# Kernel tuning notes

Hardware: AMD Instinct MI355X
Metric: run time of the kernel (lower is better)

Reference implementation:

```python
import jax, jax.numpy as jnp
import numpy as np

H = 12           # num_heads
D_MODEL = 768
SCALE = (D_MODEL // H) ** -0.5  # qk_scale default: head_dim**-0.5


def _attn_mask(q, k, v, mask):
    # sim: (b, i, j); mask broadcast over query dim (mask.unsqueeze(1) in torch)
    sim = jnp.einsum('bid,bjd->bij', q, k) + mask[:, None, :]
    a = jax.nn.softmax(sim, axis=-1)
    return jnp.einsum('bij,bjd->bid', a, v)


def setup_inputs() -> dict:
    key = jax.random.key(0)
    k0, k1, k2, k3 = jax.random.split(key, 4)
    B, F, n, D = 16, 8, 196, 768
    N = 1 + F * n  # cls + frames*patches = 1569
    x = jax.random.normal(k0, (B, N, D), jnp.float32)
    x_mask = jax.random.normal(k1, (B, N), jnp.float32)  # additive attention mask
    Wqkv = jax.random.normal(k2, (3 * D, D), jnp.float32) * (D ** -0.5)
    Wproj = jax.random.normal(k3, (D, D), jnp.float32) * (D ** -0.5)
    bproj = jnp.zeros((D,), jnp.float32)
    return {"x": x, "x_mask": x_mask, "Wqkv": Wqkv, "Wproj": Wproj,
            "bproj": bproj, "f": F}


def reference(x, x_mask, Wqkv, Wproj, bproj, f):
    B, N, D = x.shape
    h = H
    d = D // h
    # qkv projection (qkv_bias=False), split into q,k,v
    qkv = x @ Wqkv.T                       # (B, N, 3D)
    q, k, v = jnp.split(qkv, 3, axis=-1)

    def to_heads(t):  # 'b n (h d) -> (b h) n d'
        return t.reshape(B, N, h, d).transpose(0, 2, 1, 3).reshape(B * h, N, d)

    q, k, v = map(to_heads, (q, k, v))
    mask = jnp.repeat(x_mask, h, axis=0)   # repeat_interleave over heads: (B*h, N)

    q = q * SCALE
    cls_q, q_ = q[:, :1], q[:, 1:]
    cls_k, k_ = k[:, :1], k[:, 1:]
    cls_v, v_ = v[:, :1], v[:, 1:]
    cls_mask, mask_ = mask[:, :1], mask[:, 1:]

    # cls token attends to everything
    cls_out = _attn_mask(cls_q, k, v, mask)            # (B*h, 1, d)

    # spatial attention: 'b (f n) d -> (b f) n d'
    n = (N - 1) // f
    q_ = q_.reshape(B * h * f, n, d)
    k_ = k_.reshape(B * h * f, n, d)
    v_ = v_.reshape(B * h * f, n, d)
    mask_ = mask_.reshape(B * h * f, n)

    # prepend cls k/v/mask to every frame group (r = f)
    cls_k = jnp.repeat(cls_k, f, axis=0)               # (B*h*f, 1, d)
    cls_v = jnp.repeat(cls_v, f, axis=0)
    cls_m = jnp.repeat(cls_mask, f, axis=0)            # (B*h*f, 1)
    k_ = jnp.concatenate([cls_k, k_], axis=1)          # (B*h*f, n+1, d)
    v_ = jnp.concatenate([cls_v, v_], axis=1)
    m2 = jnp.concatenate([cls_m, mask_], axis=1)       # (B*h*f, n+1)

    out = _attn_mask(q_, k_, v_, m2)                   # (B*h*f, n, d)
    out = out.reshape(B * h, f * n, d)                 # '(b f) n d -> b (f n) d'
    out = jnp.concatenate([cls_out, out], axis=1)      # (B*h, N, d)
    out = out.reshape(B, h, N, d).transpose(0, 2, 1, 3).reshape(B, N, D)
    return out @ Wproj.T + bproj
```

## Files before the change

### kernel.cpp

```cpp
#include <hip/hip_runtime.h>
#include <hip/hip_bf16.h>
#include <stdint.h>

#define Hh 12
#define Dm 768
#define Bb 16
#define Nt 1569
#define Ff 8
#define NC 196
#define BH 192
#define Mr 25104
#define CPW 224
#define VTW (8*CPW)
#define PLD 232
#define CLD 132

typedef __attribute__((ext_vector_type(8))) short bf16x8;
typedef __attribute__((ext_vector_type(4))) float f32x4;

typedef const __attribute__((address_space(1))) uint32_t guint;
typedef __attribute__((address_space(3))) uint32_t luint;

static __device__ __forceinline__ float bf2f(unsigned short u) {
  union { unsigned int i; float f; } v; v.i = ((unsigned int)u) << 16; return v.f;
}
static __device__ __forceinline__ unsigned short f2bf(float f) {
  __hip_bfloat16 h = __float2bfloat16(f);
  return __builtin_bit_cast(unsigned short, h);
}

__global__ void cast3_k(const float4* __restrict__ s0, ushort4* __restrict__ d0, int n0,
                        const float4* __restrict__ s1, ushort4* __restrict__ d1, int n1,
                        const float4* __restrict__ s2, ushort4* __restrict__ d2, int n2) {
  int nTot = n0 + n1 + n2;
  for (int i = blockIdx.x * blockDim.x + threadIdx.x; i < nTot; i += gridDim.x * blockDim.x) {
    const float4* s; ushort4* d; int off;
    if (i < n0) { s = s0; d = d0; off = i; }
    else if (i < n0 + n1) { s = s1; d = d1; off = i - n0; }
    else { s = s2; d = d2; off = i - n0 - n1; }
    float4 f = s[off];
    ushort4 u;
    u.x = f2bf(f.x); u.y = f2bf(f.y); u.z = f2bf(f.z); u.w = f2bf(f.w);
    d[off] = u;
  }
}

template<int MODE>
__global__ __launch_bounds__(256) void gemm_k(
    const __hip_bfloat16* __restrict__ A,
    const __hip_bfloat16* __restrict__ W,
    int M, int K,
    __hip_bfloat16* __restrict__ qh, __hip_bfloat16* __restrict__ kh,
    __hip_bfloat16* __restrict__ vT, __hip_bfloat16* __restrict__ vcls,
    const float* __restrict__ bias, float* __restrict__ outp)
{
  __shared__ __align__(16) unsigned short shmem[128 * CLD];
  unsigned short* ls0 = shmem;
  unsigned short* ls1 = shmem + 4096;
  unsigned short* ls2 = shmem + 8192;
  unsigned short* ls3 = shmem + 12288;

  const int tid = threadIdx.x;
  const int lane = tid & 63, wid = tid >> 6;
  const int waveM = wid >> 1, waveN = wid & 1;

  const int gridN = gridDim.x;
  const int nwg = gridDim.x * gridDim.y;
  int bid = blockIdx.y * gridN + blockIdx.x;
  int q8 = nwg >> 3, r8 = nwg & 7;
  int xcd = bid & 7, lid = bid >> 3;
  int swz = (xcd < r8 ? xcd * (q8 + 1) : r8 * (q8 + 1) + (xcd - r8) * q8) + lid;
  const int mBase = (swz / gridN) * 128, nBase = (swz % gridN) * 128;

  const int l15 = lane & 15, lg = lane >> 4;
  f32x4 acc[4][4] = {};
  const int nkt = K >> 6;
  for (int kt = 0; kt < nkt; ++kt) {
#pragma unroll
    for (int s = 0; s < 2; ++s) {
      int seg = s * 256 + tid;
      int row = seg >> 2, ks = seg & 3;
      int arow = mBase + row; if (arow >= M) arow = M - 1;
      int brow = nBase + row;
      const __hip_bfloat16* ap = A + (size_t)arow * K + kt * 64 + ks * 8;
      const __hip_bfloat16* wp = W + (size_t)brow * K + kt * 64 + ks * 8;
      __builtin_amdgcn_global_load_lds((guint*)ap,        (luint*)&ls0[seg * 8], 16, 0, 0);
      __builtin_amdgcn_global_load_lds((guint*)wp,        (luint*)&ls1[seg * 8], 16, 0, 0);
      __builtin_amdgcn_global_load_lds((guint*)(ap + 32), (luint*)&ls2[seg * 8], 16, 0, 0);
      __builtin_amdgcn_global_load_lds((guint*)(wp + 32), (luint*)&ls3[seg * 8], 16, 0, 0);
    }
    __syncthreads();
    bf16x8 aF[4], bF[4], aG[4], bG[4];
#pragma unroll
    for (int i = 0; i < 4; ++i) {
      int ro = (waveM * 64 + i * 16 + l15) * 32 + lg * 8;
      int co = (waveN * 64 + i * 16 + l15) * 32 + lg * 8;
      aF[i] = *reinterpret_cast<const bf16x8*>(&ls0[ro]);
      bF[i] = *reinterpret_cast<const bf16x8*>(&ls1[co]);
      aG[i] = *reinterpret_cast<const bf16x8*>(&ls2[ro]);
      bG[i] = *reinterpret_cast<const bf16x8*>(&ls3[co]);
    }
#pragma unroll
    for (int mi = 0; mi < 4; ++mi)
#pragma unroll
      for (int ni = 0; ni < 4; ++ni) {
        acc[mi][ni] = __builtin_amdgcn_mfma_f32_16x16x32_bf16(aF[mi], bF[ni], acc[mi][ni], 0, 0, 0);
        acc[mi][ni] = __builtin_amdgcn_mfma_f32_16x16x32_bf16(aG[mi], bG[ni], acc[mi][ni], 0, 0, 0);
      }
    __syncthreads();
  }

  if (MODE == 1) {
    const bool fullM = (mBase + 128 <= M);
#pragma unroll
    for (int mi = 0; mi < 4; ++mi)
#pragma unroll
      for (int ni = 0; ni < 4; ++ni)
#pragma unroll
        for (int r = 0; r < 4; ++r) {
          int grow = mBase + waveM * 64 + mi * 16 + lg * 4 + r;
          if (!fullM && grow >= M) continue;
          int gcol = nBase + waveN * 64 + ni * 16 + l15;
          outp[(size_t)grow * Dm + gcol] = acc[mi][ni][r] + bias[gcol];
        }
    return;
  }

  const int which = nBase / Dm;
  const int headBase = (nBase - which * Dm) >> 6;
  const float scl = (which == 0) ? 0.125f : 1.f;
  const bool fullM = (mBase + 128 <= M);

  if (fullM) {
    if (which < 2) {
#pragma unroll
      for (int mi = 0; mi < 4; ++mi)
#pragma unroll
        for (int ni = 0; ni < 4; ++ni)
#pragma unroll
          for (int r = 0; r < 4; ++r)
            shmem[(waveM * 64 + mi * 16 + lg * 4 + r) * CLD + (waveN * 64 + ni * 16 + l15)]
                = f2bf(acc[mi][ni][r] * scl);
      __syncthreads();
      __hip_bfloat16* dst = (which == 0) ? qh : kh;
      int row = tid >> 1, h = tid & 1;
      int grow = mBase + row;
      int b = grow / Nt, i = grow - b * Nt;
      const uint2* sp = reinterpret_cast<const uint2*>(&shmem[row * CLD + h * 64]);
      uint2* dp = reinterpret_cast<uint2*>(
          dst + ((size_t)(b * Hh + headBase + h) * Nt + i) * 64);
#pragma unroll
      for (int j = 0; j < 16; ++j) dp[j] = sp[j];
    } else {
#pragma unroll
      for (int mi = 0; mi < 4; ++mi)
#pragma unroll
        for (int ni = 0; ni < 4; ++ni)
#pragma unroll
          for (int r = 0; r < 4; ++r)
            shmem[(waveN * 64 + ni * 16 + l15) * CLD + (waveM * 64 + mi * 16 + lg * 4 + r)]
                = f2bf(acc[mi][ni][r]);
      __syncthreads();
      int lc = tid & 127, rhalf = tid >> 7;
      int h = lc >> 6, dc = lc & 63;
      int head = headBase + h;
#pragma unroll
      for (int g = 0; g < 8; ++g) {
        int row0 = rhalf * 64 + g * 8;
        int grow0 = mBase + row0;
        int b = grow0 / Nt, i0 = grow0 - b * Nt;
        const unsigned short* sp = &shmem[lc * CLD + row0];
        if (i0 >= 1 && i0 + 8 <= Nt) {
          int j0 = i0 - 1, cc = j0 / NC, key = j0 - cc * NC;
          if (key + 8 <= NC) {
            int bh = b * Hh + head;
            __hip_bfloat16* p = vT + ((size_t)bh * 64 + dc) * VTW + cc * CPW + key;
            if ((key & 1) == 0) {
              const unsigned int* s4 = reinterpret_cast<const unsigned int*>(sp);
              unsigned int* d4 = reinterpret_cast<unsigned int*>(p);
              d4[0] = s4[0]; d4[1] = s4[1]; d4[2] = s4[2]; d4[3] = s4[3];
            } else {
#pragma unroll
              for (int j = 0; j < 8; ++j)
                p[j] = __builtin_bit_cast(__hip_bfloat16, sp[j]);
            }
            continue;
          }
        }
#pragma unroll
        for (int j = 0; j < 8; ++j) {
          int grow = grow0 + j;
          int bb = grow / Nt, ii = grow - bb * Nt;
          int bh2 = bb * Hh + head;
          unsigned short val = sp[j];
          if (ii == 0) {
            vcls[bh2 * 64 + dc] = __builtin_bit_cast(__hip_bfloat16, val);
          } else {
            int jj = ii - 1, cc2 = jj / NC, k2 = jj - cc2 * NC;
            vT[((size_t)bh2 * 64 + dc) * VTW + cc2 * CPW + k2]
                = __builtin_bit_cast(__hip_bfloat16, val);
          }
        }
      }
    }
  } else {
#pragma unroll
    for (int mi = 0; mi < 4; ++mi)
#pragma unroll
      for (int ni = 0; ni < 4; ++ni)
#pragma unroll
        for (int r = 0; r < 4; ++r) {
          int grow = mBase + waveM * 64 + mi * 16 + lg * 4 + r;
          if (grow >= M) continue;
          int gcol = nBase + waveN * 64 + ni * 16 + l15;
          float v = acc[mi][ni][r];
          int b = grow / Nt, i = grow - b * Nt;
          int hcol = gcol - which * Dm;
          int head = hcol >> 6, dc = hcol & 63;
          int bh = b * Hh + head;
          if (which == 0) {
            qh[((size_t)bh * Nt + i) * 64 + dc] = __float2bfloat16(v * 0.125f);
          } else if (which == 1) {
            kh[((size_t)bh * Nt + i) * 64 + dc] = __float2bfloat16(v);
          } else {
            if (i == 0) vcls[bh * 64 + dc] = __float2bfloat16(v);
            else {
              int j = i - 1; int cc = j / NC, key = j - cc * NC;
              vT[((size_t)bh * 64 + dc) * VTW + cc * CPW + key] = __float2bfloat16(v);
            }
          }
        }
  }
}

__global__ __launch_bounds__(256, 2) void attn_k(
    const __hip_bfloat16* __restrict__ qh, const __hip_bfloat16* __restrict__ kh,
    const __hip_bfloat16* __restrict__ vT, const __hip_bfloat16* __restrict__ vcls,
    const float* __restrict__ x_mask, __hip_bfloat16* __restrict__ ao)
{
  __shared__ __align__(16) char smem[56320];

  const int bidx = blockIdx.x;
  const int tid = threadIdx.x;

  if (bidx < BH) {
    float* sS = reinterpret_cast<float*>(smem);
    float* qv = reinterpret_cast<float*>(smem + 6400);
    float* red = reinterpret_cast<float*>(smem + 6656);
    const int bh = bidx, b = bh / Hh, head = bh - b * Hh;
    if (tid < 64) qv[tid] = __bfloat162float(qh[((size_t)bh * Nt) * 64 + tid]);
    __syncthreads();
    float lmax = -1e30f;
    for (int j = tid; j < Nt; j += 256) {
      const __hip_bfloat16* kr = kh + ((size_t)bh * Nt + j) * 64;
      float dot = 0.f;
#pragma unroll
      for (int d0 = 0; d0 < 64; d0 += 8) {
        bf16x8 kv = *reinterpret_cast<const bf16x8*>(kr + d0);
#pragma unroll
        for (int i = 0; i < 8; ++i) dot += qv[d0 + i] * bf2f((unsigned short)kv[i]);
      }
      float s = dot + x_mask[b * Nt + j];
      sS[j] = s;
      lmax = fmaxf(lmax, s);
    }
    red[tid] = lmax; __syncthreads();
    for (int off = 128; off > 0; off >>= 1) {
      if (tid < off) red[tid] = fmaxf(red[tid], red[tid + off]);
      __syncthreads();
    }
    float m = red[0]; __syncthreads();
    float lsum = 0.f;
    for (int j = tid; j < Nt; j += 256) { float e = __expf(sS[j] - m); sS[j] = e; lsum += e; }
    red[tid] = lsum; __syncthreads();
    for (int off = 128; off > 0; off >>= 1) {
      if (tid < off) red[tid] += red[tid + off];
      __syncthreads();
    }
    float rden = 1.f / red[0]; __syncthreads();
    int dc = tid & 63, part = tid >> 6;
    float partial = 0.f;
    if (part == 0) partial = sS[0] * __bfloat162float(vcls[bh * 64 + dc]);
    const __hip_bfloat16* vrow = vT + ((size_t)bh * 64 + dc) * VTW;
    for (int cc = part * 2; cc < part * 2 + 2; ++cc) {
      int base = 1 + cc * NC;
      const __hip_bfloat16* vc2 = vrow + cc * CPW;
      int key = 0;
      for (; key + 8 <= NC; key += 8) {
        bf16x8 vv = *reinterpret_cast<const bf16x8*>(vc2 + key);
#pragma unroll
        for (int i = 0; i < 8; ++i)
          partial += sS[base + key + i] * bf2f((unsigned short)vv[i]);
      }
      for (; key < NC; ++key)
        partial += sS[base + key] * __bfloat162float(vc2[key]);
    }
    red[tid] = partial; __syncthreads();
    if (tid < 64) {
      float o = (red[tid] + red[tid + 64] + red[tid + 128] + red[tid + 192]) * rden;
      ao[((size_t)b * Nt) * Dm + head * 64 + dc] = __float2bfloat16(o);
    }
    return;
  }

  __hip_bfloat16* ldsK = reinterpret_cast<__hip_bfloat16*>(smem);
  __hip_bfloat16* ldsP = reinterpret_cast<__hip_bfloat16*>(smem + 26624);

  const int g = bidx - BH;
  const int bh = g >> 3, c = g & 7;
  const int b = bh / Hh, head = bh - b * Hh;
  const int lane = tid & 63, wid = tid >> 6;
  const int l15 = lane & 15, lg = lane >> 4;

  const int kbase = 1 + c * NC;

#pragma unroll
  for (int it = 0; it < 7; ++it) {
    int idx = it * 256 + tid;
    if (idx < 1664) {
      int row = idx >> 3, c16 = idx & 7;
      int token = kbase + row; if (token > Nt - 1) token = Nt - 1;
      __builtin_amdgcn_global_load_lds(
          (guint*)(kh + ((size_t)bh * Nt + token) * 64 + ((c16 ^ (row & 7)) * 8)),
          (luint*)&ldsK[idx * 8], 16, 0, 0);
    }
  }
  __syncthreads();

  __hip_bfloat16* myP = ldsP + wid * (16 * PLD);

  const __hip_bfloat16* kc = kh + (size_t)bh * Nt * 64;
  bf16x8 ck0 = *reinterpret_cast<const bf16x8*>(kc + lg * 8);
  bf16x8 ck1 = *reinterpret_cast<const bf16x8*>(kc + 32 + lg * 8);
  const float maskCls = x_mask[b * Nt];

  for (int rt = wid; rt < 13; rt += 4) {
    int qlrow = rt * 16 + l15;
    int qtok = 1 + c * NC + qlrow; if (qtok > Nt - 1) qtok = Nt - 1;
    const __hip_bfloat16* qp = qh + ((size_t)bh * Nt + qtok) * 64;
    bf16x8 aQ0 = *reinterpret_cast<const bf16x8*>(qp + lg * 8);
    bf16x8 aQ1 = *reinterpret_cast<const bf16x8*>(qp + 32 + lg * 8);

    float pc0 = 0.f;
#pragma unroll
    for (int i = 0; i < 8; ++i)
      pc0 += bf2f((unsigned short)aQ0[i]) * bf2f((unsigned short)ck0[i])
           + bf2f((unsigned short)aQ1[i]) * bf2f((unsigned short)ck1[i]);
    pc0 += __shfl_xor(pc0, 16);
    pc0 += __shfl_xor(pc0, 32);
    pc0 += maskCls;

    f32x4 S[13];
    float mv[13];
#define LD_MM(i) { \
    int row = (i) * 16 + l15; \
    bf16x8 kb0 = *reinterpret_cast<const bf16x8*>(&ldsK[row * 64 + ((lg ^ (l15 & 7)) * 8)]); \
    bf16x8 kb1 = *reinterpret_cast<const bf16x8*>(&ldsK[row * 64 + (((4 + lg) ^ (l15 & 7)) * 8)]); \
    mv[i] = (row < NC) ? x_mask[b * Nt + kbase + row] : -1e30f; \
    f32x4 sa = {}; \
    sa = __builtin_amdgcn_mfma_f32_16x16x32_bf16(aQ0, kb0, sa, 0, 0, 0); \
    sa = __builtin_amdgcn_mfma_f32_16x16x32_bf16(aQ1, kb1, sa, 0, 0, 0); \
    S[i][0] = sa[0] + mv[i]; S[i][1] = sa[1] + mv[i]; \
    S[i][2] = sa[2] + mv[i]; S[i][3] = sa[3] + mv[i]; }
    LD_MM(0) LD_MM(1) LD_MM(2) LD_MM(3) LD_MM(4) LD_MM(5) LD_MM(6)
    LD_MM(7) LD_MM(8) LD_MM(9) LD_MM(10) LD_MM(11) LD_MM(12)
#undef LD_MM

    float pcls[4], rden[4];
#pragma unroll
    for (int r = 0; r < 4; ++r) {
      float m = -1e30f;
#pragma unroll
      for (int nt = 0; nt < 13; ++nt) m = fmaxf(m, S[nt][r]);
      m = fmaxf(m, __shfl_xor(m, 1));
      m = fmaxf(m, __shfl_xor(m, 2));
      m = fmaxf(m, __shfl_xor(m, 4));
      m = fmaxf(m, __shfl_xor(m, 8));
      float sc = __shfl(pc0, lg * 4 + r);
      m = fmaxf(m, sc);
      float sum = 0.f;
#pragma unroll
      for (int nt = 0; nt < 13; ++nt) { float e = __expf(S[nt][r] - m); S[nt][r] = e; sum += e; }
      sum += __shfl_xor(sum, 1);
      sum += __shfl_xor(sum, 2);
      sum += __shfl_xor(sum, 4);
      sum += __shfl_xor(sum, 8);
      float pc = __expf(sc - m);
      pcls[r] = pc;
      rden[r] = 1.f / (sum + pc);
    }

#pragma unroll
    for (int nt = 0; nt < 13; ++nt)
#pragma unroll
      for (int r = 0; r < 4; ++r)
        myP[(lg * 4 + r) * PLD + nt * 16 + l15] = __float2bfloat16(S[nt][r]);
#pragma unroll
    for (int r = 0; r < 4; ++r)
      myP[l15 * PLD + 208 + lg * 4 + r] = __float2bfloat16(0.f);
    asm volatile("s_waitcnt lgkmcnt(0)" ::: "memory");
    __builtin_amdgcn_sched_barrier(0);

    f32x4 O[4] = {};
#define PVK(kt) { \
    bf16x8 aP = *reinterpret_cast<const bf16x8*>(&myP[l15 * PLD + (kt) * 32 + lg * 8]); \
    { int dc = 0 * 16 + l15; bf16x8 bV = *reinterpret_cast<const bf16x8*>(vT + ((size_t)bh * 64 + dc) * VTW + c * CPW + (kt) * 32 + lg * 8); \
      O[0] = __builtin_amdgcn_mfma_f32_16x16x32_bf16(aP, bV, O[0], 0, 0, 0); } \
    { int dc = 1 * 16 + l15; bf16x8 bV = *reinterpret_cast<const bf16x8*>(vT + ((size_t)bh * 64 + dc) * VTW + c * CPW + (kt) * 32 + lg * 8); \
      O[1] = __builtin_amdgcn_mfma_f32_16x16x32_bf16(aP, bV, O[1], 0, 0, 0); } \
    { int dc = 2 * 16 + l15; bf16x8 bV = *reinterpret_cast<const bf16x8*>(vT + ((size_t)bh * 64 + dc) * VTW + c * CPW + (kt) * 32 + lg * 8); \
      O[2] = __builtin_amdgcn_mfma_f32_16x16x32_bf16(aP, bV, O[2], 0, 0, 0); } \
    { int dc = 3 * 16 + l15; bf16x8 bV = *reinterpret_cast<const bf16x8*>(vT + ((size_t)bh * 64 + dc) * VTW + c * CPW + (kt) * 32 + lg * 8); \
      O[3] = __builtin_amdgcn_mfma_f32_16x16x32_bf16(aP, bV, O[3], 0, 0, 0); } }
    PVK(0) PVK(1) PVK(2) PVK(3) PVK(4) PVK(5) PVK(6)
#undef PVK

#pragma unroll
    for (int ni = 0; ni < 4; ++ni) {
      int dc = ni * 16 + l15;
      float vc = __bfloat162float(vcls[bh * 64 + dc]);
#pragma unroll
      for (int r = 0; r < 4; ++r) {
        int lrow = rt * 16 + lg * 4 + r;
        if (lrow < NC) {
          float o = (O[ni][r] + pcls[r] * vc) * rden[r];
          int tok = 1 + c * NC + lrow;
          ao[((size_t)b * Nt + tok) * Dm + head * 64 + dc] = __float2bfloat16(o);
        }
      }
    }
  }
}

extern "C" void kernel_launch(void* const* d_in, const int* in_sizes, int n_in,
                              void* d_out, int out_size, void* d_ws, size_t ws_size,
                              hipStream_t stream) {
  const float* x     = (const float*)d_in[0];
  const float* xmask = (const float*)d_in[1];
  const float* wqkv  = (const float*)d_in[2];
  const float* wproj = (const float*)d_in[3];
  const float* bproj = (const float*)d_in[4];
  float* outp = (float*)d_out;

  char* ws = (char*)d_ws;
  size_t off = 0;
  auto alloc = [&](size_t bytes) {
    char* p = ws + off;
    off += (bytes + 255) & ~(size_t)255;
    return p;
  };
  __hip_bfloat16* xb     = (__hip_bfloat16*)alloc((size_t)Mr * Dm * 2);
  __hip_bfloat16* wqkvb  = (__hip_bfloat16*)alloc((size_t)3 * Dm * Dm * 2);
  __hip_bfloat16* wprojb = (__hip_bfloat16*)alloc((size_t)Dm * Dm * 2);
  __hip_bfloat16* qh     = (__hip_bfloat16*)alloc((size_t)BH * Nt * 64 * 2);
  __hip_bfloat16* kh     = (__hip_bfloat16*)alloc((size_t)BH * Nt * 64 * 2);
  __hip_bfloat16* vT     = (__hip_bfloat16*)alloc((size_t)BH * 64 * VTW * 2);
  __hip_bfloat16* vcls   = (__hip_bfloat16*)alloc((size_t)BH * 64 * 2);
  __hip_bfloat16* ao = xb;

  cast3_k<<<2048, 256, 0, stream>>>((const float4*)x, (ushort4*)xb, Mr * Dm / 4,
                                    (const float4*)wqkv, (ushort4*)wqkvb, 3 * Dm * Dm / 4,
                                    (const float4*)wproj, (ushort4*)wprojb, Dm * Dm / 4);

  gemm_k<0><<<dim3(18, 197), 256, 0, stream>>>(xb, wqkvb, Mr, Dm, qh, kh, vT, vcls, nullptr, nullptr);

  attn_k<<<BH + BH * Ff, 256, 0, stream>>>(qh, kh, vT, vcls, xmask, ao);

  gemm_k<1><<<dim3(6, 197), 256, 0, stream>>>(ao, wprojb, Mr, Dm, nullptr, nullptr, nullptr, nullptr, bproj, outp);
}
```

Baseline: 351.9 us.

## Stage V tile in swizzled LDS and widen attention blocks to 512 threads

The attention kernel now runs 512 threads per block (8 waves), so the 13 query row tiles per frame group are spread over 8 waves instead of 4, and the CLS path reduces over 8 partial groups. Each block also copies its frame's V^T tile (64 x 224) into LDS with an XOR swizzle, and the PV MFMA B-operand loads read from LDS instead of global memory. This aims to raise parallelism per block and remove repeated global loads of V across waves. In exchange, LDS per block grows to about 116 KB, which likely allows only one block per CU. Waves 5-7 get a single row tile while the others get two, leaving the work unbalanced.

```diff
diff --git a/kernel.cpp b/kernel.cpp
--- a/kernel.cpp
+++ b/kernel.cpp
@@ -233,12 +233,12 @@
   }
 }
 
-__global__ __launch_bounds__(256, 2) void attn_k(
+__global__ __launch_bounds__(512, 2) void attn_k(
     const __hip_bfloat16* __restrict__ qh, const __hip_bfloat16* __restrict__ kh,
     const __hip_bfloat16* __restrict__ vT, const __hip_bfloat16* __restrict__ vcls,
     const float* __restrict__ x_mask, __hip_bfloat16* __restrict__ ao)
 {
-  __shared__ __align__(16) char smem[56320];
+  __shared__ __align__(16) char smem[118784];
 
   const int bidx = blockIdx.x;
   const int tid = threadIdx.x;
@@ -251,7 +251,7 @@
     if (tid < 64) qv[tid] = __bfloat162float(qh[((size_t)bh * Nt) * 64 + tid]);
     __syncthreads();
     float lmax = -1e30f;
-    for (int j = tid; j < Nt; j += 256) {
+    for (int j = tid; j < Nt; j += 512) {
       const __hip_bfloat16* kr = kh + ((size_t)bh * Nt + j) * 64;
       float dot = 0.f;
 #pragma unroll
@@ -265,15 +265,15 @@
       lmax = fmaxf(lmax, s);
     }
     red[tid] = lmax; __syncthreads();
-    for (int off = 128; off > 0; off >>= 1) {
+    for (int off = 256; off > 0; off >>= 1) {
       if (tid < off) red[tid] = fmaxf(red[tid], red[tid + off]);
       __syncthreads();
     }
     float m = red[0]; __syncthreads();
     float lsum = 0.f;
-    for (int j = tid; j < Nt; j += 256) { float e = __expf(sS[j] - m); sS[j] = e; lsum += e; }
+    for (int j = tid; j < Nt; j += 512) { float e = __expf(sS[j] - m); sS[j] = e; lsum += e; }
     red[tid] = lsum; __syncthreads();
-    for (int off = 128; off > 0; off >>= 1) {
+    for (int off = 256; off > 0; off >>= 1) {
       if (tid < off) red[tid] += red[tid + off];
       __syncthreads();
     }
@@ -281,10 +281,9 @@
     int dc = tid & 63, part = tid >> 6;
     float partial = 0.f;
     if (part == 0) partial = sS[0] * __bfloat162float(vcls[bh * 64 + dc]);
-    const __hip_bfloat16* vrow = vT + ((size_t)bh * 64 + dc) * VTW;
-    for (int cc = part * 2; cc < part * 2 + 2; ++cc) {
-      int base = 1 + cc * NC;
-      const __hip_bfloat16* vc2 = vrow + cc * CPW;
+    {
+      int base = 1 + part * NC;
+      const __hip_bfloat16* vc2 = vT + ((size_t)bh * 64 + dc) * VTW + part * CPW;
       int key = 0;
       for (; key + 8 <= NC; key += 8) {
         bf16x8 vv = *reinterpret_cast<const bf16x8*>(vc2 + key);
@@ -297,14 +296,17 @@
     }
     red[tid] = partial; __syncthreads();
     if (tid < 64) {
-      float o = (red[tid] + red[tid + 64] + red[tid + 128] + red[tid + 192]) * rden;
-      ao[((size_t)b * Nt) * Dm + head * 64 + dc] = __float2bfloat16(o);
+      float o = 0.f;
+#pragma unroll
+      for (int k = 0; k < 8; ++k) o += red[tid + 64 * k];
+      ao[((size_t)b * Nt) * Dm + head * 64 + dc] = __float2bfloat16(o * rden);
     }
     return;
   }
 
   __hip_bfloat16* ldsK = reinterpret_cast<__hip_bfloat16*>(smem);
-  __hip_bfloat16* ldsP = reinterpret_cast<__hip_bfloat16*>(smem + 26624);
+  __hip_bfloat16* ldsV = reinterpret_cast<__hip_bfloat16*>(smem + 26624);
+  __hip_bfloat16* ldsP = reinterpret_cast<__hip_bfloat16*>(smem + 59392);
 
   const int g = bidx - BH;
   const int bh = g >> 3, c = g & 7;
@@ -315,8 +317,8 @@
   const int kbase = 1 + c * NC;
 
 #pragma unroll
-  for (int it = 0; it < 7; ++it) {
-    int idx = it * 256 + tid;
+  for (int it = 0; it < 4; ++it) {
+    int idx = it * 512 + tid;
     if (idx < 1664) {
       int row = idx >> 3, c16 = idx & 7;
       int token = kbase + row; if (token > Nt - 1) token = Nt - 1;
@@ -325,6 +327,16 @@
           (luint*)&ldsK[idx * 8], 16, 0, 0);
     }
   }
+#pragma unroll
+  for (int it = 0; it < 4; ++it) {
+    int idx = it * 512 + tid;
+    if (idx < 1792) {
+      int dc = idx / 28, u = idx - dc * 28;
+      uint4 v = *reinterpret_cast<const uint4*>(
+          vT + ((size_t)bh * 64 + dc) * VTW + c * CPW + u * 8);
+      *reinterpret_cast<uint4*>(&ldsV[dc * 256 + ((u ^ (dc & 7)) * 8)]) = v;
+    }
+  }
   __syncthreads();
 
   __hip_bfloat16* myP = ldsP + wid * (16 * PLD);
@@ -334,7 +346,7 @@
   bf16x8 ck1 = *reinterpret_cast<const bf16x8*>(kc + 32 + lg * 8);
   const float maskCls = x_mask[b * Nt];
 
-  for (int rt = wid; rt < 13; rt += 4) {
+  for (int rt = wid; rt < 13; rt += 8) {
     int qlrow = rt * 16 + l15;
     int qtok = 1 + c * NC + qlrow; if (qtok > Nt - 1) qtok = Nt - 1;
     const __hip_bfloat16* qp = qh + ((size_t)bh * Nt + qtok) * 64;
@@ -404,13 +416,13 @@
     f32x4 O[4] = {};
 #define PVK(kt) { \
     bf16x8 aP = *reinterpret_cast<const bf16x8*>(&myP[l15 * PLD + (kt) * 32 + lg * 8]); \
-    { int dc = 0 * 16 + l15; bf16x8 bV = *reinterpret_cast<const bf16x8*>(vT + ((size_t)bh * 64 + dc) * VTW + c * CPW + (kt) * 32 + lg * 8); \
+    { int dc = 0 * 16 + l15; bf16x8 bV = *reinterpret_cast<const bf16x8*>(&ldsV[dc * 256 + ((((kt) * 4 + lg) ^ (l15 & 7)) * 8)]); \
       O[0] = __builtin_amdgcn_mfma_f32_16x16x32_bf16(aP, bV, O[0], 0, 0, 0); } \
-    { int dc = 1 * 16 + l15; bf16x8 bV = *reinterpret_cast<const bf16x8*>(vT + ((size_t)bh * 64 + dc) * VTW + c * CPW + (kt) * 32 + lg * 8); \
+    { int dc = 1 * 16 + l15; bf16x8 bV = *reinterpret_cast<const bf16x8*>(&ldsV[dc * 256 + ((((kt) * 4 + lg) ^ (l15 & 7)) * 8)]); \
       O[1] = __builtin_amdgcn_mfma_f32_16x16x32_bf16(aP, bV, O[1], 0, 0, 0); } \
-    { int dc = 2 * 16 + l15; bf16x8 bV = *reinterpret_cast<const bf16x8*>(vT + ((size_t)bh * 64 + dc) * VTW + c * CPW + (kt) * 32 + lg * 8); \
+    { int dc = 2 * 16 + l15; bf16x8 bV = *reinterpret_cast<const bf16x8*>(&ldsV[dc * 256 + ((((kt) * 4 + lg) ^ (l15 & 7)) * 8)]); \
       O[2] = __builtin_amdgcn_mfma_f32_16x16x32_bf16(aP, bV, O[2], 0, 0, 0); } \
-    { int dc = 3 * 16 + l15; bf16x8 bV = *reinterpret_cast<const bf16x8*>(vT + ((size_t)bh * 64 + dc) * VTW + c * CPW + (kt) * 32 + lg * 8); \
+    { int dc = 3 * 16 + l15; bf16x8 bV = *reinterpret_cast<const bf16x8*>(&ldsV[dc * 256 + ((((kt) * 4 + lg) ^ (l15 & 7)) * 8)]); \
       O[3] = __builtin_amdgcn_mfma_f32_16x16x32_bf16(aP, bV, O[3], 0, 0, 0); } }
     PVK(0) PVK(1) PVK(2) PVK(3) PVK(4) PVK(5) PVK(6)
 #undef PVK
@@ -464,7 +476,7 @@
 
   gemm_k<0><<<dim3(18, 197), 256, 0, stream>>>(xb, wqkvb, Mr, Dm, qh, kh, vT, vcls, nullptr, nullptr);
 
-  attn_k<<<BH + BH * Ff, 256, 0, stream>>>(qh, kh, vT, vcls, xmask, ao);
+  attn_k<<<BH + BH * Ff, 512, 0, stream>>>(qh, kh, vT, vcls, xmask, ao);
 
   gemm_k<1><<<dim3(6, 197), 256, 0, stream>>>(ao, wprojb, Mr, Dm, nullptr, nullptr, nullptr, nullptr, bproj, outp);
 }
```

New measurement: 300.2 us (median of 2 runs). 14.7% less time.
